# Optimization experiments

Hardware: AMD Instinct MI355X
Metric: run time of the kernel (lower is better)

## Reference

```python
import jax, jax.numpy as jnp
import numpy as np

B, D, E, H, O, TOPK = 16384, 256, 8, 128, 1, 2
THRESHOLD = 0.5
NUM_SCALES = 3
TAUS = np.linspace(5.0, 20.0, NUM_SCALES)  # MSLIFNeuron tau_range=(5,20), num_scales=3


def setup_inputs() -> dict:
    key = jax.random.key(0)
    ks = jax.random.split(key, 10)
    s = lambda fan: 1.0 / np.sqrt(fan)
    return {
        "features": jax.random.normal(ks[0], (B, D), jnp.float32),
        "Wg": jax.random.normal(ks[1], (D, E), jnp.float32) * s(D),
        "W1": jax.random.normal(ks[2], (E, D, H), jnp.float32) * s(D),
        "b1": jnp.zeros((E, H), jnp.float32),
        "Wp": jax.random.normal(ks[3], (E, H, H), jnp.float32) * s(H),
        "bp": jnp.zeros((E, H), jnp.float32),
        "mix_logit": jnp.zeros((E,), jnp.float32),
        "Wo": jax.random.normal(ks[4], (E, H, O), jnp.float32) * s(H),
        "bo": jnp.zeros((E, O), jnp.float32),
    }


def _mslif_spikes(x):
    # multi-scale LIF, single step from zero state: v_s = x * (1 - exp(-dt/tau_s))
    decays = jnp.asarray(1.0 - np.exp(-1.0 / TAUS), x.dtype)  # [S]
    v = x[:, None, :] * decays[None, :, None]                  # [B,S,D]
    return (v > THRESHOLD).astype(x.dtype).mean(axis=1)        # [B,D]


def reference(features, Wg, W1, b1, Wp, bp, mix_logit, Wo, bo):
    # gating: softmax over experts, top-k renormalized
    gate = jax.nn.softmax(features @ Wg, axis=-1)              # [B,E]
    _, idx = jax.lax.top_k(gate, TOPK)                         # [B,K]
    mask = jax.nn.one_hot(idx, E, dtype=gate.dtype).sum(1)     # [B,E]
    w = gate * mask
    w = w / (w.sum(-1, keepdims=True) + 1e-10)

    # spike generator (computed in expert forward; not used downstream)
    _spikes = _mslif_spikes(features)

    # NeuroDynArch expert: static core + plasticity mix
    core = jax.nn.relu(jnp.einsum('bd,edh->beh', features, W1) + b1[None])
    plast = jnp.tanh(jnp.einsum('beh,ehk->bek', core, Wp) + bp[None])
    mix = jax.nn.sigmoid(mix_logit)[None, :, None]             # [1,E,1]
    mixed = core * (1.0 - mix) + plast * mix                   # [B,E,H]
    out_e = jnp.einsum('beh,eho->beo', mixed, Wo) + bo[None]   # [B,E,O]
    return jnp.einsum('beo,be->bo', out_e, w)                  # [B,O]
```

## Files before the change

kernel.cpp:

```cpp
#include <hip/hip_runtime.h>

#define BB 16384
#define DD 256
#define EE 8
#define HH 128

typedef __attribute__((ext_vector_type(8))) short short8;
typedef __attribute__((ext_vector_type(4))) float f32x4;

__device__ __forceinline__ ushort f2bf(float f){
    const unsigned u = __float_as_uint(f);
    return (ushort)((u + 0x7fffu + ((u >> 16) & 1u)) >> 16);
}
__device__ __forceinline__ float bf2f(ushort s){
    return __uint_as_float(((unsigned)s) << 16);
}
__device__ __forceinline__ float fast_tanh(float v){
    v = fminf(fmaxf(v, -15.0f), 15.0f);
    const float a = __expf(2.0f * v);
    return (a - 1.0f) / (a + 1.0f);
}

__global__ __launch_bounds__(256) void transpose_kernel(
    const float* __restrict__ W1, const float* __restrict__ Wp,
    ushort* __restrict__ W1t, ushort* __restrict__ Wpt, int* __restrict__ counts)
{
    __shared__ float tile[64 * 68];
    int b = blockIdx.x;
    const int t = threadIdx.x;
    if (b == 0 && t < EE) counts[t] = 0;
    const float* src; ushort* dst; int K;
    int k0, h0;
    if (b < 64){
        const int e = b >> 3, kt = (b >> 1) & 3, ht = b & 1;
        src = W1 + (size_t)e * DD * HH;  dst = W1t + (size_t)e * HH * DD;
        K = DD; k0 = kt * 64; h0 = ht * 64;
    } else {
        b -= 64;
        const int e = b >> 2, kt = (b >> 1) & 1, ht = b & 1;
        src = Wp + (size_t)e * HH * HH;  dst = Wpt + (size_t)e * HH * HH;
        K = HH; k0 = kt * 64; h0 = ht * 64;
    }
    #pragma unroll
    for (int j = 0; j < 4; j++){
        const int idx = t + 256 * j;
        const int kk = idx >> 4, hh = (idx & 15) * 4;
        const float4 v = *(const float4*)(src + (size_t)(k0 + kk) * HH + h0 + hh);
        *(float4*)&tile[kk * 68 + hh] = v;
    }
    __syncthreads();
    #pragma unroll
    for (int j = 0; j < 4; j++){
        const int idx = t + 256 * j;
        const int hh = idx >> 4, kk = (idx & 15) * 4;
        ushort4 o;
        o.x = f2bf(tile[(kk + 0) * 68 + hh]);
        o.y = f2bf(tile[(kk + 1) * 68 + hh]);
        o.z = f2bf(tile[(kk + 2) * 68 + hh]);
        o.w = f2bf(tile[(kk + 3) * 68 + hh]);
        *(ushort4*)&dst[(size_t)(h0 + hh) * K + k0 + kk] = o;
    }
}

__global__ __launch_bounds__(256) void routing_kernel(
    const float* __restrict__ x, const float* __restrict__ Wg,
    int* __restrict__ counts, int* __restrict__ rowids, float* __restrict__ wgts,
    float* __restrict__ out)
{
    __shared__ __align__(16) float WgT[EE][DD];
    __shared__ int   le[64];
    __shared__ float lw[64];
    __shared__ int   loff[64];
    __shared__ int   lcount[EE];
    __shared__ int   lbase[EE];

    const int t = threadIdx.x;
    const int rowBase = blockIdx.x * 32;
    if (t < 32) out[rowBase + t] = 0.0f;
    {
        const float4* g = (const float4*)(Wg + t * EE);
        const float4 a = g[0], b = g[1];
        WgT[0][t] = a.x; WgT[1][t] = a.y; WgT[2][t] = a.z; WgT[3][t] = a.w;
        WgT[4][t] = b.x; WgT[5][t] = b.y; WgT[6][t] = b.z; WgT[7][t] = b.w;
    }
    if (t < EE) lcount[t] = 0;
    __syncthreads();

    const int lane = t & 63;
    const int wid  = t >> 6;

    for (int it = 0; it < 8; it++){
        const int slot = wid * 8 + it;
        const int row  = rowBase + slot;
        const float4 xv = *(const float4*)(x + row * DD + lane * 4);
        float p[EE];
        #pragma unroll
        for (int e = 0; e < EE; e++){
            const float4 w = *(const float4*)&WgT[e][lane * 4];
            p[e] = xv.x * w.x + xv.y * w.y + xv.z * w.z + xv.w * w.w;
        }
        #pragma unroll
        for (int off = 32; off >= 1; off >>= 1){
            #pragma unroll
            for (int e = 0; e < EE; e++) p[e] += __shfl_down(p[e], off, 64);
        }
        if (lane == 0){
            int e0 = 0; float l0 = p[0];
            #pragma unroll
            for (int e = 1; e < EE; e++){ if (p[e] > l0){ l0 = p[e]; e0 = e; } }
            int e1 = -1; float l1 = -3.0e38f;
            #pragma unroll
            for (int e = 0; e < EE; e++){ if (e != e0 && p[e] > l1){ l1 = p[e]; e1 = e; } }
            const float tt  = __expf(l1 - l0);
            const float inv = 1.0f / (1.0f + tt);
            le[slot]      = e0;  lw[slot]      = inv;
            le[32 + slot] = e1;  lw[32 + slot] = tt * inv;
        }
    }
    __syncthreads();
    if (t < 64) loff[t] = atomicAdd(&lcount[le[t]], 1);
    __syncthreads();
    if (t < EE) lbase[t] = atomicAdd(&counts[t], lcount[t]);
    __syncthreads();
    if (t < 64){
        const int e   = le[t];
        const int pos = lbase[e] + loff[t];
        rowids[e * BB + pos] = rowBase + (t & 31);
        wgts[e * BB + pos]   = lw[t];
    }
}

#define XS_S 264
#define CS_S 136

__global__ __launch_bounds__(256, 2) void expert_kernel(
    const float* __restrict__ x,
    const ushort* __restrict__ W1t, const float* __restrict__ b1,
    const ushort* __restrict__ Wpt, const float* __restrict__ bp,
    const float* __restrict__ mix_logit,
    const float* __restrict__ Wo, const float* __restrict__ bo,
    const int* __restrict__ counts, const int* __restrict__ rowids,
    const float* __restrict__ wgts, float* __restrict__ out)
{
    const int me    = blockIdx.y;
    const int cnt   = counts[me];
    const int start = blockIdx.x * 64;
    if (start >= cnt) return;

    __shared__ ushort Xs[64 * XS_S];
    __shared__ ushort coreS[64 * CS_S];
    __shared__ int   rid_s[64];
    __shared__ float w_s[64];

    const int t = threadIdx.x;
    if (t < 64){
        const int idx = start + t;
        if (idx < cnt){ rid_s[t] = rowids[me * BB + idx]; w_s[t] = wgts[me * BB + idx]; }
        else          { rid_s[t] = 0;                     w_s[t] = 0.0f; }
    }
    __syncthreads();

    #pragma unroll
    for (int j = 0; j < 16; j++){
        const int idx = t + 256 * j;
        const int r  = idx >> 6;
        const int kq = (idx & 63) << 2;
        const float4 v = *(const float4*)(x + (size_t)rid_s[r] * DD + kq);
        ushort4 bv;
        bv.x = f2bf(v.x); bv.y = f2bf(v.y); bv.z = f2bf(v.z); bv.w = f2bf(v.w);
        *(ushort4*)&Xs[r * XS_S + kq] = bv;
    }
    __syncthreads();

    const int lane = t & 63;
    const int w    = t >> 6;
    const int m16  = lane & 15;
    const int q    = lane >> 4;
    const int r0   = 32 * (w >> 1);
    const int c0   = 64 * (w & 1);

    f32x4 acc[2][4];
    #pragma unroll
    for (int ct = 0; ct < 4; ct++){
        const float bj = b1[me * HH + c0 + ct * 16 + m16];
        #pragma unroll
        for (int rt = 0; rt < 2; rt++) acc[rt][ct] = (f32x4){bj, bj, bj, bj};
    }
    const ushort* W1te = W1t + (size_t)me * HH * DD;
    #pragma unroll
    for (int ks = 0; ks < 8; ks++){
        const int k0 = ks * 32;
        short8 af[2], bf[4];
        #pragma unroll
        for (int rt = 0; rt < 2; rt++)
            af[rt] = *(const short8*)&Xs[(r0 + rt * 16 + m16) * XS_S + k0 + q * 8];
        #pragma unroll
        for (int ct = 0; ct < 4; ct++)
            bf[ct] = *(const short8*)&W1te[(size_t)(c0 + ct * 16 + m16) * DD + k0 + q * 8];
        #pragma unroll
        for (int rt = 0; rt < 2; rt++)
            #pragma unroll
            for (int ct = 0; ct < 4; ct++)
                acc[rt][ct] = __builtin_amdgcn_mfma_f32_16x16x32_bf16(af[rt], bf[ct], acc[rt][ct], 0, 0, 0);
    }

    #pragma unroll
    for (int rt = 0; rt < 2; rt++)
        #pragma unroll
        for (int ct = 0; ct < 4; ct++)
            #pragma unroll
            for (int j = 0; j < 4; j++){
                const int row = r0 + rt * 16 + q * 4 + j;
                const int col = c0 + ct * 16 + m16;
                coreS[row * CS_S + col] = f2bf(fmaxf(acc[rt][ct][j], 0.0f));
            }
    __syncthreads();

    #pragma unroll
    for (int ct = 0; ct < 4; ct++){
        const float bj = bp[me * HH + c0 + ct * 16 + m16];
        #pragma unroll
        for (int rt = 0; rt < 2; rt++) acc[rt][ct] = (f32x4){bj, bj, bj, bj};
    }
    const ushort* Wpte = Wpt + (size_t)me * HH * HH;
    #pragma unroll
    for (int ks = 0; ks < 4; ks++){
        const int k0 = ks * 32;
        short8 af[2], bf[4];
        #pragma unroll
        for (int rt = 0; rt < 2; rt++)
            af[rt] = *(const short8*)&coreS[(r0 + rt * 16 + m16) * CS_S + k0 + q * 8];
        #pragma unroll
        for (int ct = 0; ct < 4; ct++)
            bf[ct] = *(const short8*)&Wpte[(size_t)(c0 + ct * 16 + m16) * HH + k0 + q * 8];
        #pragma unroll
        for (int rt = 0; rt < 2; rt++)
            #pragma unroll
            for (int ct = 0; ct < 4; ct++)
                acc[rt][ct] = __builtin_amdgcn_mfma_f32_16x16x32_bf16(af[rt], bf[ct], acc[rt][ct], 0, 0, 0);
    }

    const float mv  = 1.0f / (1.0f + __expf(-mix_logit[me]));
    const float om  = 1.0f - mv;
    const float bov = bo[me];
    float wo[4];
    #pragma unroll
    for (int ct = 0; ct < 4; ct++) wo[ct] = Wo[me * HH + c0 + ct * 16 + m16];

    float red[2][4];
    #pragma unroll
    for (int rt = 0; rt < 2; rt++)
        #pragma unroll
        for (int j = 0; j < 4; j++){
            float s = 0.0f;
            const int row = r0 + rt * 16 + q * 4 + j;
            #pragma unroll
            for (int ct = 0; ct < 4; ct++){
                const int col = c0 + ct * 16 + m16;
                const float pl = fast_tanh(acc[rt][ct][j]);
                const float cv = bf2f(coreS[row * CS_S + col]);
                s = fmaf(om * cv + mv * pl, wo[ct], s);
            }
            red[rt][j] = s;
        }
    #pragma unroll
    for (int off = 8; off >= 1; off >>= 1)
        #pragma unroll
        for (int rt = 0; rt < 2; rt++)
            #pragma unroll
            for (int j = 0; j < 4; j++)
                red[rt][j] += __shfl_xor(red[rt][j], off, 64);

    if (m16 == 0){
        const float bb = (c0 == 0) ? bov : 0.0f;
        #pragma unroll
        for (int rt = 0; rt < 2; rt++)
            #pragma unroll
            for (int j = 0; j < 4; j++){
                const int row = r0 + rt * 16 + q * 4 + j;
                const float ww = w_s[row];
                if (ww != 0.0f) atomicAdd(&out[rid_s[row]], (red[rt][j] + bb) * ww);
            }
    }
}

extern "C" void kernel_launch(void* const* d_in, const int* in_sizes, int n_in,
                              void* d_out, int out_size, void* d_ws, size_t ws_size,
                              hipStream_t stream) {
    (void)in_sizes; (void)n_in; (void)out_size; (void)ws_size;
    const float* x   = (const float*)d_in[0];
    const float* Wg  = (const float*)d_in[1];
    const float* W1  = (const float*)d_in[2];
    const float* b1  = (const float*)d_in[3];
    const float* Wp  = (const float*)d_in[4];
    const float* bp  = (const float*)d_in[5];
    const float* ml  = (const float*)d_in[6];
    const float* Wo  = (const float*)d_in[7];
    const float* bo  = (const float*)d_in[8];
    float* out = (float*)d_out;

    char* ws = (char*)d_ws;
    int*    counts = (int*)ws;
    int*    rowids = (int*)(ws + 256);
    float*  wgts   = (float*)(ws + 256 + (size_t)EE * BB * 4);
    ushort* W1t    = (ushort*)(ws + 256 + 2 * (size_t)EE * BB * 4);
    ushort* Wpt    = W1t + (size_t)EE * HH * DD;

    transpose_kernel<<<96, 256, 0, stream>>>(W1, Wp, W1t, Wpt, counts);
    routing_kernel<<<BB / 32, 256, 0, stream>>>(x, Wg, counts, rowids, wgts, out);
    expert_kernel<<<dim3(BB / 64, EE), 256, 0, stream>>>(
        x, W1t, b1, Wpt, bp, ml, Wo, bo, counts, rowids, wgts, out);
}
```

Measured before the change: 118.9 us.

## Precast features to bf16 in routing and gather via direct global-to-LDS loads

The routing kernel now writes a bf16 copy of the features while it already has them in registers. The expert kernel then gathers its rows from this half-size copy with global_load_lds (direct global-to-LDS DMA) into an XOR-swizzled unpadded tile, and the MFMA A-fragment reads use the matching swizzle. This removes the per-expert fp32 gather-and-convert, which was repeated for each of the top-2 experts, and halves the gather bytes. In exchange, routing now writes an extra 8 MB bf16 buffer, and the swizzle indexing has to line up with the order in which the 16-byte LDS loads land.

```diff
diff --git a/kernel.cpp b/kernel.cpp
--- a/kernel.cpp
+++ b/kernel.cpp
@@ -19,6 +19,11 @@
     v = fminf(fmaxf(v, -15.0f), 15.0f);
     const float a = __expf(2.0f * v);
     return (a - 1.0f) / (a + 1.0f);
+}
+__device__ __forceinline__ void gload_lds16(const void* g, void* l){
+    __builtin_amdgcn_global_load_lds(
+        (const __attribute__((address_space(1))) unsigned*)g,
+        (__attribute__((address_space(3))) unsigned*)l, 16, 0, 0);
 }
 
 __global__ __launch_bounds__(256) void transpose_kernel(
@@ -65,7 +70,7 @@
 __global__ __launch_bounds__(256) void routing_kernel(
     const float* __restrict__ x, const float* __restrict__ Wg,
     int* __restrict__ counts, int* __restrict__ rowids, float* __restrict__ wgts,
-    float* __restrict__ out)
+    float* __restrict__ out, ushort* __restrict__ xbf)
 {
     __shared__ __align__(16) float WgT[EE][DD];
     __shared__ int   le[64];
@@ -93,6 +98,11 @@
         const int slot = wid * 8 + it;
         const int row  = rowBase + slot;
         const float4 xv = *(const float4*)(x + row * DD + lane * 4);
+        {
+            ushort4 o;
+            o.x = f2bf(xv.x); o.y = f2bf(xv.y); o.z = f2bf(xv.z); o.w = f2bf(xv.w);
+            *(ushort4*)&xbf[(size_t)row * DD + lane * 4] = o;
+        }
         float p[EE];
         #pragma unroll
         for (int e = 0; e < EE; e++){
@@ -130,11 +140,10 @@
     }
 }
 
-#define XS_S 264
 #define CS_S 136
 
 __global__ __launch_bounds__(256, 2) void expert_kernel(
-    const float* __restrict__ x,
+    const ushort* __restrict__ xbf,
     const ushort* __restrict__ W1t, const float* __restrict__ b1,
     const ushort* __restrict__ Wpt, const float* __restrict__ bp,
     const float* __restrict__ mix_logit,
@@ -147,7 +156,7 @@
     const int start = blockIdx.x * 64;
     if (start >= cnt) return;
 
-    __shared__ ushort Xs[64 * XS_S];
+    __shared__ ushort Xs[64 * DD];
     __shared__ ushort coreS[64 * CS_S];
     __shared__ int   rid_s[64];
     __shared__ float w_s[64];
@@ -160,24 +169,28 @@
     }
     __syncthreads();
 
-    #pragma unroll
-    for (int j = 0; j < 16; j++){
-        const int idx = t + 256 * j;
-        const int r  = idx >> 6;
-        const int kq = (idx & 63) << 2;
-        const float4 v = *(const float4*)(x + (size_t)rid_s[r] * DD + kq);
-        ushort4 bv;
-        bv.x = f2bf(v.x); bv.y = f2bf(v.y); bv.z = f2bf(v.z); bv.w = f2bf(v.w);
-        *(ushort4*)&Xs[r * XS_S + kq] = bv;
-    }
-    __syncthreads();
-
     const int lane = t & 63;
     const int w    = t >> 6;
+
+    {
+        const int rsub = lane >> 5;
+        const int c    = lane & 31;
+        #pragma unroll
+        for (int i = 0; i < 8; i++){
+            const int row = w * 16 + i * 2 + rsub;
+            const int sc  = c ^ (row & 7);
+            const ushort* gp = xbf + (size_t)rid_s[row] * DD + sc * 8;
+            gload_lds16(gp, &Xs[(w * 16 + i * 2) * DD]);
+        }
+    }
+    asm volatile("s_waitcnt vmcnt(0)" ::: "memory");
+    __syncthreads();
+
     const int m16  = lane & 15;
     const int q    = lane >> 4;
     const int r0   = 32 * (w >> 1);
     const int c0   = 64 * (w & 1);
+    const int swz  = m16 & 7;
 
     f32x4 acc[2][4];
     #pragma unroll
@@ -189,14 +202,14 @@
     const ushort* W1te = W1t + (size_t)me * HH * DD;
     #pragma unroll
     for (int ks = 0; ks < 8; ks++){
-        const int k0 = ks * 32;
+        const int kc = ks * 4 + q;
         short8 af[2], bf[4];
         #pragma unroll
         for (int rt = 0; rt < 2; rt++)
-            af[rt] = *(const short8*)&Xs[(r0 + rt * 16 + m16) * XS_S + k0 + q * 8];
+            af[rt] = *(const short8*)&Xs[(r0 + rt * 16 + m16) * DD + ((kc ^ swz) * 8)];
         #pragma unroll
         for (int ct = 0; ct < 4; ct++)
-            bf[ct] = *(const short8*)&W1te[(size_t)(c0 + ct * 16 + m16) * DD + k0 + q * 8];
+            bf[ct] = *(const short8*)&W1te[(size_t)(c0 + ct * 16 + m16) * DD + ks * 32 + q * 8];
         #pragma unroll
         for (int rt = 0; rt < 2; rt++)
             #pragma unroll
@@ -305,9 +318,10 @@
     float*  wgts   = (float*)(ws + 256 + (size_t)EE * BB * 4);
     ushort* W1t    = (ushort*)(ws + 256 + 2 * (size_t)EE * BB * 4);
     ushort* Wpt    = W1t + (size_t)EE * HH * DD;
+    ushort* xbf    = Wpt + (size_t)EE * HH * HH;
 
     transpose_kernel<<<96, 256, 0, stream>>>(W1, Wp, W1t, Wpt, counts);
-    routing_kernel<<<BB / 32, 256, 0, stream>>>(x, Wg, counts, rowids, wgts, out);
+    routing_kernel<<<BB / 32, 256, 0, stream>>>(x, Wg, counts, rowids, wgts, out, xbf);
     expert_kernel<<<dim3(BB / 64, EE), 256, 0, stream>>>(
-        x, W1t, b1, Wpt, bp, ml, Wo, bo, counts, rowids, wgts, out);
-}
+        xbf, W1t, b1, Wpt, bp, ml, Wo, bo, counts, rowids, wgts, out);
+}
```

Result: no change. 120.2 us (+1.1%).

## Compute all experts densely per row block, fusing routing and expert passes

Applied to the files above, without the earlier changes.

Replaces the scatter-based top-2 dispatch (row lists, atomics, separate routing and expert kernels) with a single fused kernel. Each 32-row block computes gating and then evaluates every expert, weighting by the gate (zero for unselected experts). This removes the gather of inputs, the global atomics, the counts reset and a launch, at the cost of doing four times the expert matmul work. Output is written directly without atomics.

```diff
diff --git a/kernel.cpp b/kernel.cpp
--- a/kernel.cpp
+++ b/kernel.cpp
@@ -4,6 +4,9 @@
 #define DD 256
 #define EE 8
 #define HH 128
+#define TBLK 96
+#define XS_S 264
+#define CS_S 136
 
 typedef __attribute__((ext_vector_type(8))) short short8;
 typedef __attribute__((ext_vector_type(4))) float f32x4;
@@ -21,14 +24,13 @@
     return (a - 1.0f) / (a + 1.0f);
 }
 
-__global__ __launch_bounds__(256) void transpose_kernel(
+__global__ __launch_bounds__(256) void prep_kernel(
     const float* __restrict__ W1, const float* __restrict__ Wp,
-    ushort* __restrict__ W1t, ushort* __restrict__ Wpt, int* __restrict__ counts)
+    ushort* __restrict__ W1t, ushort* __restrict__ Wpt)
 {
     __shared__ float tile[64 * 68];
     int b = blockIdx.x;
     const int t = threadIdx.x;
-    if (b == 0 && t < EE) counts[t] = 0;
     const float* src; ushort* dst; int K;
     int k0, h0;
     if (b < 64){
@@ -62,42 +64,60 @@
     }
 }
 
-__global__ __launch_bounds__(256) void routing_kernel(
+__global__ __launch_bounds__(512, 4) void dense_kernel(
     const float* __restrict__ x, const float* __restrict__ Wg,
-    int* __restrict__ counts, int* __restrict__ rowids, float* __restrict__ wgts,
-    float* __restrict__ out)
+    const ushort* __restrict__ W1t, const float* __restrict__ b1,
+    const ushort* __restrict__ Wpt, const float* __restrict__ bp,
+    const float* __restrict__ mix_logit, const float* __restrict__ Wo,
+    const float* __restrict__ bo, float* __restrict__ out)
 {
     __shared__ __align__(16) float WgT[EE][DD];
-    __shared__ int   le[64];
-    __shared__ float lw[64];
-    __shared__ int   loff[64];
-    __shared__ int   lcount[EE];
-    __shared__ int   lbase[EE];
+    __shared__ ushort Xs[32 * XS_S];
+    __shared__ ushort coreS[32 * CS_S];
+    __shared__ int    le[64];
+    __shared__ float  lw[64];
+    __shared__ float  wES[32];
+    __shared__ float  redS[4][32];
+    __shared__ float  mvS[EE], boS[EE];
 
     const int t = threadIdx.x;
     const int rowBase = blockIdx.x * 32;
-    if (t < 32) out[rowBase + t] = 0.0f;
-    {
+    const int lane = t & 63;
+    const int wid  = t >> 6;
+
+    if (t < 256){
         const float4* g = (const float4*)(Wg + t * EE);
         const float4 a = g[0], b = g[1];
         WgT[0][t] = a.x; WgT[1][t] = a.y; WgT[2][t] = a.z; WgT[3][t] = a.w;
         WgT[4][t] = b.x; WgT[5][t] = b.y; WgT[6][t] = b.z; WgT[7][t] = b.w;
     }
-    if (t < EE) lcount[t] = 0;
-    __syncthreads();
-
-    const int lane = t & 63;
-    const int wid  = t >> 6;
-
-    for (int it = 0; it < 8; it++){
-        const int slot = wid * 8 + it;
+    if (t < EE){ mvS[t] = 1.0f / (1.0f + __expf(-mix_logit[t])); boS[t] = bo[t]; }
+
+    #pragma unroll
+    for (int i = 0; i < 2; i++){
+        const int c   = t * 2 + i;
+        const int row = c >> 5, cc = c & 31;
+        const float* xp = x + (size_t)(rowBase + row) * DD + cc * 8;
+        const float4 v0 = *(const float4*)xp;
+        const float4 v1 = *(const float4*)(xp + 4);
+        short8 o;
+        o[0] = (short)f2bf(v0.x); o[1] = (short)f2bf(v0.y);
+        o[2] = (short)f2bf(v0.z); o[3] = (short)f2bf(v0.w);
+        o[4] = (short)f2bf(v1.x); o[5] = (short)f2bf(v1.y);
+        o[6] = (short)f2bf(v1.z); o[7] = (short)f2bf(v1.w);
+        *(short8*)&Xs[row * XS_S + cc * 8] = o;
+    }
+    __syncthreads();
+
+    for (int it = 0; it < 4; it++){
+        const int slot = wid * 4 + it;
         const int row  = rowBase + slot;
-        const float4 xv = *(const float4*)(x + row * DD + lane * 4);
+        const float4 xv = *(const float4*)(x + (size_t)row * DD + lane * 4);
         float p[EE];
         #pragma unroll
         for (int e = 0; e < EE; e++){
-            const float4 w = *(const float4*)&WgT[e][lane * 4];
-            p[e] = xv.x * w.x + xv.y * w.y + xv.z * w.z + xv.w * w.w;
+            const float4 ww = *(const float4*)&WgT[e][lane * 4];
+            p[e] = xv.x * ww.x + xv.y * ww.y + xv.z * ww.z + xv.w * ww.w;
         }
         #pragma unroll
         for (int off = 32; off >= 1; off >>= 1){
@@ -118,170 +138,99 @@
         }
     }
     __syncthreads();
-    if (t < 64) loff[t] = atomicAdd(&lcount[le[t]], 1);
-    __syncthreads();
-    if (t < EE) lbase[t] = atomicAdd(&counts[t], lcount[t]);
-    __syncthreads();
-    if (t < 64){
-        const int e   = le[t];
-        const int pos = lbase[e] + loff[t];
-        rowids[e * BB + pos] = rowBase + (t & 31);
-        wgts[e * BB + pos]   = lw[t];
-    }
-}
-
-#define XS_S 264
-#define CS_S 136
-
-__global__ __launch_bounds__(256, 2) void expert_kernel(
-    const float* __restrict__ x,
-    const ushort* __restrict__ W1t, const float* __restrict__ b1,
-    const ushort* __restrict__ Wpt, const float* __restrict__ bp,
-    const float* __restrict__ mix_logit,
-    const float* __restrict__ Wo, const float* __restrict__ bo,
-    const int* __restrict__ counts, const int* __restrict__ rowids,
-    const float* __restrict__ wgts, float* __restrict__ out)
-{
-    const int me    = blockIdx.y;
-    const int cnt   = counts[me];
-    const int start = blockIdx.x * 64;
-    if (start >= cnt) return;
-
-    __shared__ ushort Xs[64 * XS_S];
-    __shared__ ushort coreS[64 * CS_S];
-    __shared__ int   rid_s[64];
-    __shared__ float w_s[64];
-
-    const int t = threadIdx.x;
-    if (t < 64){
-        const int idx = start + t;
-        if (idx < cnt){ rid_s[t] = rowids[me * BB + idx]; w_s[t] = wgts[me * BB + idx]; }
-        else          { rid_s[t] = 0;                     w_s[t] = 0.0f; }
-    }
-    __syncthreads();
-
-    #pragma unroll
-    for (int j = 0; j < 16; j++){
-        const int idx = t + 256 * j;
-        const int r  = idx >> 6;
-        const int kq = (idx & 63) << 2;
-        const float4 v = *(const float4*)(x + (size_t)rid_s[r] * DD + kq);
-        ushort4 bv;
-        bv.x = f2bf(v.x); bv.y = f2bf(v.y); bv.z = f2bf(v.z); bv.w = f2bf(v.w);
-        *(ushort4*)&Xs[r * XS_S + kq] = bv;
-    }
-    __syncthreads();
-
-    const int lane = t & 63;
-    const int w    = t >> 6;
-    const int m16  = lane & 15;
-    const int q    = lane >> 4;
-    const int r0   = 32 * (w >> 1);
-    const int c0   = 64 * (w & 1);
-
-    f32x4 acc[2][4];
-    #pragma unroll
-    for (int ct = 0; ct < 4; ct++){
-        const float bj = b1[me * HH + c0 + ct * 16 + m16];
-        #pragma unroll
-        for (int rt = 0; rt < 2; rt++) acc[rt][ct] = (f32x4){bj, bj, bj, bj};
-    }
-    const ushort* W1te = W1t + (size_t)me * HH * DD;
-    #pragma unroll
-    for (int ks = 0; ks < 8; ks++){
-        const int k0 = ks * 32;
-        short8 af[2], bf[4];
-        #pragma unroll
-        for (int rt = 0; rt < 2; rt++)
-            af[rt] = *(const short8*)&Xs[(r0 + rt * 16 + m16) * XS_S + k0 + q * 8];
-        #pragma unroll
-        for (int ct = 0; ct < 4; ct++)
-            bf[ct] = *(const short8*)&W1te[(size_t)(c0 + ct * 16 + m16) * DD + k0 + q * 8];
-        #pragma unroll
-        for (int rt = 0; rt < 2; rt++)
-            #pragma unroll
-            for (int ct = 0; ct < 4; ct++)
-                acc[rt][ct] = __builtin_amdgcn_mfma_f32_16x16x32_bf16(af[rt], bf[ct], acc[rt][ct], 0, 0, 0);
-    }
-
-    #pragma unroll
-    for (int rt = 0; rt < 2; rt++)
-        #pragma unroll
-        for (int ct = 0; ct < 4; ct++)
-            #pragma unroll
-            for (int j = 0; j < 4; j++){
-                const int row = r0 + rt * 16 + q * 4 + j;
+
+    const int m16   = lane & 15;
+    const int q     = lane >> 4;
+    const int rhalf = wid >> 2;
+    const int cq    = wid & 3;
+    const int r0    = rhalf * 16;
+    const int c0    = cq * 32;
+
+    float red[4] = {0.0f, 0.0f, 0.0f, 0.0f};
+
+    #pragma unroll 1
+    for (int e = 0; e < EE; e++){
+        if (t < 32)
+            wES[t] = (le[t] == e) ? lw[t] : ((le[32 + t] == e) ? lw[32 + t] : 0.0f);
+
+        f32x4 acc[2];
+        #pragma unroll
+        for (int ct = 0; ct < 2; ct++){
+            const float bj = b1[e * HH + c0 + ct * 16 + m16];
+            acc[ct] = (f32x4){bj, bj, bj, bj};
+        }
+        const ushort* W1te = W1t + (size_t)e * HH * DD;
+        #pragma unroll
+        for (int ks = 0; ks < 8; ks++){
+            const short8 af = *(const short8*)&Xs[(r0 + m16) * XS_S + ks * 32 + q * 8];
+            #pragma unroll
+            for (int ct = 0; ct < 2; ct++){
+                const short8 bfr = *(const short8*)&W1te[(size_t)(c0 + ct * 16 + m16) * DD + ks * 32 + q * 8];
+                acc[ct] = __builtin_amdgcn_mfma_f32_16x16x32_bf16(af, bfr, acc[ct], 0, 0, 0);
+            }
+        }
+        #pragma unroll
+        for (int ct = 0; ct < 2; ct++)
+            #pragma unroll
+            for (int j = 0; j < 4; j++)
+                coreS[(r0 + q * 4 + j) * CS_S + c0 + ct * 16 + m16] =
+                    f2bf(fmaxf(acc[ct][j], 0.0f));
+        __syncthreads();
+
+        f32x4 acc2[2];
+        #pragma unroll
+        for (int ct = 0; ct < 2; ct++){
+            const float bj = bp[e * HH + c0 + ct * 16 + m16];
+            acc2[ct] = (f32x4){bj, bj, bj, bj};
+        }
+        const ushort* Wpte = Wpt + (size_t)e * HH * HH;
+        #pragma unroll
+        for (int ks = 0; ks < 4; ks++){
+            const short8 af2 = *(const short8*)&coreS[(r0 + m16) * CS_S + ks * 32 + q * 8];
+            #pragma unroll
+            for (int ct = 0; ct < 2; ct++){
+                const short8 bfr = *(const short8*)&Wpte[(size_t)(c0 + ct * 16 + m16) * HH + ks * 32 + q * 8];
+                acc2[ct] = __builtin_amdgcn_mfma_f32_16x16x32_bf16(af2, bfr, acc2[ct], 0, 0, 0);
+            }
+        }
+
+        const float mv   = mvS[e];
+        const float om   = 1.0f - mv;
+        const float badd = (cq == 0) ? boS[e] : 0.0f;
+        float wo[2];
+        #pragma unroll
+        for (int ct = 0; ct < 2; ct++) wo[ct] = Wo[e * HH + c0 + ct * 16 + m16];
+
+        #pragma unroll
+        for (int j = 0; j < 4; j++){
+            const int row = r0 + q * 4 + j;
+            float s = 0.0f;
+            #pragma unroll
+            for (int ct = 0; ct < 2; ct++){
                 const int col = c0 + ct * 16 + m16;
-                coreS[row * CS_S + col] = f2bf(fmaxf(acc[rt][ct][j], 0.0f));
-            }
-    __syncthreads();
-
-    #pragma unroll
-    for (int ct = 0; ct < 4; ct++){
-        const float bj = bp[me * HH + c0 + ct * 16 + m16];
-        #pragma unroll
-        for (int rt = 0; rt < 2; rt++) acc[rt][ct] = (f32x4){bj, bj, bj, bj};
-    }
-    const ushort* Wpte = Wpt + (size_t)me * HH * HH;
-    #pragma unroll
-    for (int ks = 0; ks < 4; ks++){
-        const int k0 = ks * 32;
-        short8 af[2], bf[4];
-        #pragma unroll
-        for (int rt = 0; rt < 2; rt++)
-            af[rt] = *(const short8*)&coreS[(r0 + rt * 16 + m16) * CS_S + k0 + q * 8];
-        #pragma unroll
-        for (int ct = 0; ct < 4; ct++)
-            bf[ct] = *(const short8*)&Wpte[(size_t)(c0 + ct * 16 + m16) * HH + k0 + q * 8];
-        #pragma unroll
-        for (int rt = 0; rt < 2; rt++)
-            #pragma unroll
-            for (int ct = 0; ct < 4; ct++)
-                acc[rt][ct] = __builtin_amdgcn_mfma_f32_16x16x32_bf16(af[rt], bf[ct], acc[rt][ct], 0, 0, 0);
-    }
-
-    const float mv  = 1.0f / (1.0f + __expf(-mix_logit[me]));
-    const float om  = 1.0f - mv;
-    const float bov = bo[me];
-    float wo[4];
-    #pragma unroll
-    for (int ct = 0; ct < 4; ct++) wo[ct] = Wo[me * HH + c0 + ct * 16 + m16];
-
-    float red[2][4];
-    #pragma unroll
-    for (int rt = 0; rt < 2; rt++)
-        #pragma unroll
-        for (int j = 0; j < 4; j++){
-            float s = 0.0f;
-            const int row = r0 + rt * 16 + q * 4 + j;
-            #pragma unroll
-            for (int ct = 0; ct < 4; ct++){
-                const int col = c0 + ct * 16 + m16;
-                const float pl = fast_tanh(acc[rt][ct][j]);
+                const float pl = fast_tanh(acc2[ct][j]);
                 const float cv = bf2f(coreS[row * CS_S + col]);
                 s = fmaf(om * cv + mv * pl, wo[ct], s);
             }
-            red[rt][j] = s;
-        }
+            red[j] = fmaf(wES[row], s + badd, red[j]);
+        }
+        __syncthreads();
+    }
+
     #pragma unroll
     for (int off = 8; off >= 1; off >>= 1)
         #pragma unroll
-        for (int rt = 0; rt < 2; rt++)
-            #pragma unroll
-            for (int j = 0; j < 4; j++)
-                red[rt][j] += __shfl_xor(red[rt][j], off, 64);
-
-    if (m16 == 0){
-        const float bb = (c0 == 0) ? bov : 0.0f;
-        #pragma unroll
-        for (int rt = 0; rt < 2; rt++)
-            #pragma unroll
-            for (int j = 0; j < 4; j++){
-                const int row = r0 + rt * 16 + q * 4 + j;
-                const float ww = w_s[row];
-                if (ww != 0.0f) atomicAdd(&out[rid_s[row]], (red[rt][j] + bb) * ww);
-            }
-    }
+        for (int j = 0; j < 4; j++)
+            red[j] += __shfl_xor(red[j], off, 64);
+
+    if (m16 == 0)
+        #pragma unroll
+        for (int j = 0; j < 4; j++)
+            redS[cq][r0 + q * 4 + j] = red[j];
+    __syncthreads();
+
+    if (t < 32)
+        out[rowBase + t] = redS[0][t] + redS[1][t] + redS[2][t] + redS[3][t];
 }
 
 extern "C" void kernel_launch(void* const* d_in, const int* in_sizes, int n_in,
@@ -299,15 +248,11 @@
     const float* bo  = (const float*)d_in[8];
     float* out = (float*)d_out;
 
-    char* ws = (char*)d_ws;
-    int*    counts = (int*)ws;
-    int*    rowids = (int*)(ws + 256);
-    float*  wgts   = (float*)(ws + 256 + (size_t)EE * BB * 4);
-    ushort* W1t    = (ushort*)(ws + 256 + 2 * (size_t)EE * BB * 4);
-    ushort* Wpt    = W1t + (size_t)EE * HH * DD;
-
-    transpose_kernel<<<96, 256, 0, stream>>>(W1, Wp, W1t, Wpt, counts);
-    routing_kernel<<<BB / 32, 256, 0, stream>>>(x, Wg, counts, rowids, wgts, out);
-    expert_kernel<<<dim3(BB / 64, EE), 256, 0, stream>>>(
-        x, W1t, b1, Wpt, bp, ml, Wo, bo, counts, rowids, wgts, out);
-}
+    char*   ws  = (char*)d_ws;
+    ushort* W1t = (ushort*)ws;
+    ushort* Wpt = W1t + (size_t)EE * HH * DD;
+
+    prep_kernel<<<TBLK, 256, 0, stream>>>(W1, Wp, W1t, Wpt);
+    dense_kernel<<<BB / 32, 512, 0, stream>>>(
+        x, Wg, W1t, b1, Wpt, bp, ml, Wo, bo, out);
+}
```

Result: slower. 175.3 us (+47.4%).
